# Performance work log

Hardware: AMD Instinct MI355X
Metric: run time of the kernel (lower is better)

The kernel has to match this reference:

```python
import jax, jax.numpy as jnp
import numpy as np
import math

EMBED_DIMS = 256
NUM_LANDMARKS = 40  # hard-coded k=40 in the original module
B, N = 2, 8192


def setup_inputs() -> dict:
    key = jax.random.key(0)
    ks = jax.random.split(key, 9)
    C = EMBED_DIMS
    w = lambda k: jax.random.normal(k, (C, C), dtype=jnp.float32) * 0.02
    b = lambda k: jax.random.normal(k, (C,), dtype=jnp.float32) * 0.02
    return {
        "query": jax.random.normal(ks[0], (B, N, C), dtype=jnp.float32),
        "Wq": w(ks[1]), "bq": b(ks[2]),
        "Wk": w(ks[3]), "bk": b(ks[4]),
        "Wv": w(ks[5]), "bv": b(ks[6]),
        "Wo": w(ks[7]), "bo": b(ks[8]),
    }


def reference(query, Wq, bq, Wk, bk, Wv, bv, Wo, bo):
    # key = value = identity = query (defaults in the original forward)
    C = query.shape[-1]
    scaling = math.sqrt(C)

    q = query @ Wq.T + bq  # [B, N, C]
    k = query @ Wk.T + bk
    v = query @ Wv.T + bv

    # Full similarity only to score keys: score_m[b, m] = sum_n sim_nm[b, n, m]
    sim_nm = jnp.einsum('bnc,bmc->bnm', q, k) / scaling  # [B, N, N]
    score_m = sim_nm.sum(axis=1)                          # [B, N]

    _, top_idx = jax.lax.top_k(score_m, NUM_LANDMARKS)    # [B, 40]
    selected = jnp.take_along_axis(k, top_idx[:, :, None], axis=1)  # [B, 40, C]

    sim_qn = jax.nn.softmax(jnp.einsum('bnc,bkc->bnk', q, selected) / scaling, axis=-1)  # [B, N, 40]
    sim_km = jax.nn.softmax(jnp.einsum('bmc,bkc->bmk', k, selected) / scaling, axis=-1)  # [B, N, 40]

    sim_qk = jnp.einsum('bnk,bmk->bnm', sim_qn, sim_km)   # [B, N, N]
    out = jnp.einsum('bnm,bmc->bnc', sim_qk, v)           # [B, N, C]
    out = out @ Wo.T + bo
    return query + out  # identity residual; dropouts are identity at p=0
```

## Files before the change

kernel.cpp:

```cpp
#include <hip/hip_runtime.h>
#include <cstddef>
#include <cstdint>

#define BATCH 2
#define SEQ 8192
#define CH 256
#define NLM 40
#define MROWS (BATCH * SEQ)
#define INV_SCALE 0.0625f
#define NCBLK 256

typedef unsigned short ushort_t;
typedef __attribute__((ext_vector_type(8))) short short8;
typedef __attribute__((ext_vector_type(4))) float floatx4;

__device__ __forceinline__ ushort_t f2bf(float f) {
    unsigned int u = __float_as_uint(f);
    u += 0x7FFFu + ((u >> 16) & 1u);
    return (ushort_t)(u >> 16);
}
__device__ __forceinline__ float bf2f(ushort_t u) {
    return __uint_as_float(((unsigned)u) << 16);
}

__global__ __launch_bounds__(256) void convert_colsum(const float* __restrict__ x,
                                                      ushort_t* __restrict__ xbf,
                                                      float* __restrict__ partial) {
    __shared__ float red[4][256];
    const int b = blockIdx.y;
    const int r0 = blockIdx.x * 32;
    const int t = threadIdx.x;
    const int c4 = (t & 63) * 4;
    const int rg = t >> 6;
    const float* base = x + ((size_t)b * SEQ + r0) * 256;
    ushort_t* obase = xbf + ((size_t)b * SEQ + r0) * 256;
    float4 s = {0.f, 0.f, 0.f, 0.f};
#pragma unroll
    for (int i = 0; i < 8; i++) {
        const int r = rg + i * 4;
        const float4 a = *(const float4*)&base[(size_t)r * 256 + c4];
        uint2 o;
        o.x = f2bf(a.x) | ((unsigned)f2bf(a.y) << 16);
        o.y = f2bf(a.z) | ((unsigned)f2bf(a.w) << 16);
        *(uint2*)&obase[(size_t)r * 256 + c4] = o;
        s.x += a.x; s.y += a.y; s.z += a.z; s.w += a.w;
    }
    *(float4*)&red[rg][c4] = s;
    __syncthreads();
    const float tot = red[0][t] + red[1][t] + red[2][t] + red[3][t];
    partial[((size_t)b * NCBLK + blockIdx.x) * 256 + t] = tot;
}

__global__ __launch_bounds__(1024) void ws_kernel(const float* __restrict__ partial,
                                                  const float* __restrict__ Wq,
                                                  const float* __restrict__ bq,
                                                  const float* __restrict__ Wk,
                                                  float* __restrict__ ws,
                                                  float* __restrict__ tmat) {
    const int b = blockIdx.x;
    __shared__ float xs[256];
    __shared__ float qs[256];
    __shared__ float ppart[4][256];
    const int t = threadIdx.x;
    {
        float* tz = tmat + (size_t)b * NLM * 256;
        for (int i = t; i < NLM * 256; i += 1024) tz[i] = 0.f;
    }
    {
        const int c = t & 255, qd = t >> 8;
        const float* pb = partial + ((size_t)b * NCBLK + qd * 64) * 256 + c;
        float a = 0.f;
#pragma unroll 8
        for (int i = 0; i < 64; i++) a += pb[(size_t)i * 256];
        ppart[qd][c] = a;
    }
    __syncthreads();
    if (t < 256) xs[t] = ppart[0][t] + ppart[1][t] + ppart[2][t] + ppart[3][t];
    __syncthreads();
    const int lane = t & 63, w = t >> 6;
    for (int g = 0; g < 16; g++) {
        const int o = w * 16 + g;
        const float4 wq = *(const float4*)&Wq[(size_t)o * 256 + lane * 4];
        const float4 x4 = *(const float4*)&xs[lane * 4];
        float d = wq.x * x4.x + wq.y * x4.y + wq.z * x4.z + wq.w * x4.w;
#pragma unroll
        for (int off = 32; off >= 1; off >>= 1) d += __shfl_down(d, off);
        if (lane == 0) qs[o] = d + 8192.0f * bq[o];
    }
    __syncthreads();
    const int c = t & 255, part = t >> 8;
    float a = 0.f;
    for (int o = part * 64; o < part * 64 + 64; o++)
        a += Wk[(size_t)o * 256 + c] * qs[o];
    ppart[part][c] = a;
    __syncthreads();
    if (t < 256)
        ws[b * 256 + t] = ppart[0][t] + ppart[1][t] + ppart[2][t] + ppart[3][t];
}

__global__ __launch_bounds__(256) void gemm_qkv_score(const ushort_t* __restrict__ xbf,
                                                      const float* __restrict__ Wq,
                                                      const float* __restrict__ Wk,
                                                      const float* __restrict__ Wv,
                                                      const float* __restrict__ bq,
                                                      const float* __restrict__ bk,
                                                      const float* __restrict__ bv,
                                                      ushort_t* __restrict__ qkv,
                                                      const float* __restrict__ query,
                                                      const float* __restrict__ ws,
                                                      float* __restrict__ score) {
    __shared__ __align__(16) ushort_t As[128 * 72];
    __shared__ __align__(16) ushort_t Bs[64 * 40];
    const int z = blockIdx.z;
    const int t = threadIdx.x;
    const int lane = t & 63;
    const int w = t >> 6;

    if (z == 3) {
        const int blk = blockIdx.y * 4 + blockIdx.x;
#pragma unroll
        for (int i = 0; i < 8; i++) {
            const int g = blk * 32 + i * 4 + w;
            const int b = g >> 13;
            const int m = g & 8191;
            const float4 kv = *(const float4*)&query[(size_t)g * 256 + lane * 4];
            const float4 qs = *(const float4*)&ws[b * 256 + lane * 4];
            float d = kv.x * qs.x + kv.y * qs.y + kv.z * qs.z + kv.w * qs.w;
#pragma unroll
            for (int off = 32; off >= 1; off >>= 1) d += __shfl_down(d, off);
            if (lane == 0) score[(size_t)b * SEQ + m] = d * INV_SCALE;
        }
        return;
    }

    const float* __restrict__ W = (z == 0) ? Wq : (z == 1) ? Wk : Wv;
    const float* __restrict__ bias = (z == 0) ? bq : (z == 1) ? bk : bv;
    ushort_t* __restrict__ out = qkv + (size_t)z * MROWS * 256;
    const int o0 = blockIdx.x * 64;
    const int m0 = blockIdx.y * 128;
    const int quad = lane >> 4;
    const int l16 = lane & 15;

    floatx4 acc[2][4];
#pragma unroll
    for (int rt = 0; rt < 2; rt++)
#pragma unroll
        for (int ct = 0; ct < 4; ct++) acc[rt][ct] = (floatx4){0.f, 0.f, 0.f, 0.f};

    for (int kc = 0; kc < 256; kc += 32) {
#pragma unroll
        for (int u = 0; u < 2; u++) {
            const int cid = t + u * 256;
            const int row = cid >> 2, off = cid & 3;
            *(uint4*)&As[row * 40 + off * 8] =
                *(const uint4*)&xbf[(size_t)(m0 + row) * 256 + kc + off * 8];
        }
        {
            const int row = t >> 2, off = t & 3;
            const float* wp = &W[(size_t)(o0 + row) * 256 + kc + off * 8];
            const float4 a = *(const float4*)wp;
            const float4 c = *(const float4*)(wp + 4);
            uint4 o;
            o.x = f2bf(a.x) | ((unsigned)f2bf(a.y) << 16);
            o.y = f2bf(a.z) | ((unsigned)f2bf(a.w) << 16);
            o.z = f2bf(c.x) | ((unsigned)f2bf(c.y) << 16);
            o.w = f2bf(c.z) | ((unsigned)f2bf(c.w) << 16);
            *(uint4*)&Bs[row * 40 + off * 8] = o;
        }
        __syncthreads();
        short8 a[2], b[4];
#pragma unroll
        for (int rt = 0; rt < 2; rt++)
            a[rt] = *(const short8*)&As[(w * 32 + rt * 16 + l16) * 40 + quad * 8];
#pragma unroll
        for (int ct = 0; ct < 4; ct++)
            b[ct] = *(const short8*)&Bs[(ct * 16 + l16) * 40 + quad * 8];
#pragma unroll
        for (int rt = 0; rt < 2; rt++)
#pragma unroll
            for (int ct = 0; ct < 4; ct++)
                acc[rt][ct] = __builtin_amdgcn_mfma_f32_16x16x32_bf16(
                    a[rt], b[ct], acc[rt][ct], 0, 0, 0);
        __syncthreads();
    }

#pragma unroll
    for (int rt = 0; rt < 2; rt++) {
#pragma unroll
        for (int ct = 0; ct < 4; ct++) {
            const int col = ct * 16 + l16;
            const float bb = bias[o0 + col];
#pragma unroll
            for (int reg = 0; reg < 4; reg++) {
                const int row = w * 32 + rt * 16 + quad * 4 + reg;
                As[row * 72 + col] = f2bf(acc[rt][ct][reg] + bb);
            }
        }
    }
    __syncthreads();
#pragma unroll
    for (int u = 0; u < 4; u++) {
        const int cid = t + u * 256;
        const int row = cid >> 3;
        const int off = (cid & 7) * 8;
        *(uint4*)&out[(size_t)(m0 + row) * 256 + o0 + off] =
            *(const uint4*)&As[row * 72 + off];
    }
}

__global__ __launch_bounds__(1024) void topk_gather(const float* __restrict__ score,
                                                    const ushort_t* __restrict__ kmat,
                                                    float* __restrict__ sel) {
    const int b = blockIdx.x;
    const int t = threadIdx.x;
    __shared__ unsigned hist[256];
    __shared__ unsigned wsum[64];
    __shared__ unsigned sPrefix, sMask, sRem, sNeq;
    __shared__ int sNgt;
    __shared__ int top[NLM];
    __shared__ unsigned topkey[NLM];

    unsigned key[8];
#pragma unroll
    for (int j = 0; j < 8; j++) {
        const unsigned u = __float_as_uint(score[(size_t)b * SEQ + t + j * 1024]);
        key[j] = u ^ (unsigned)(((int)u >> 31) | 0x80000000);
    }
    if (t == 0) { sPrefix = 0; sMask = 0; sRem = NLM; sNgt = 0; sNeq = 0; }

    for (int lvl = 0; lvl < 4; lvl++) {
        const int shift = 24 - 8 * lvl;
        if (t < 256) hist[t] = 0;
        __syncthreads();
        const unsigned pfx = sPrefix, msk = sMask;
#pragma unroll
        for (int j = 0; j < 8; j++)
            if (((key[j] ^ pfx) & msk) == 0)
                atomicAdd(&hist[(key[j] >> shift) & 255u], 1u);
        __syncthreads();
        if (t < 64) wsum[t] = hist[t * 4] + hist[t * 4 + 1] + hist[t * 4 + 2] + hist[t * 4 + 3];
        __syncthreads();
        if (t == 0) {
            unsigned rem = sRem, cum = 0;
            int g = 63;
            for (; g > 0; g--) { if (cum + wsum[g] >= rem) break; cum += wsum[g]; }
            int d = g * 4 + 3;
            for (; d > g * 4; d--) { if (cum + hist[d] >= rem) break; cum += hist[d]; }
            sRem = rem - cum;
            sPrefix |= ((unsigned)d) << shift;
            sMask |= 255u << shift;
        }
        __syncthreads();
    }
    const unsigned K40 = sPrefix;
    const unsigned rem = sRem;
    const int ngt = NLM - (int)rem;

#pragma unroll
    for (int j = 0; j < 8; j++) {
        if (key[j] > K40) {
            const int slot = atomicAdd(&sNgt, 1);
            top[slot] = t + j * 1024; topkey[slot] = key[j];
        } else if (key[j] == K40) {
            const unsigned e = atomicAdd(&sNeq, 1u);
            if (e < rem) {
                const int slot = ngt + (int)e;
                top[slot] = t + j * 1024; topkey[slot] = key[j];
            }
        }
    }
    __syncthreads();

    if (t < 64) {
        unsigned long long c = (t < NLM)
            ? ((((unsigned long long)(~topkey[t])) << 32) | (unsigned)top[t])
            : 0xFFFFFFFFFFFFFFFFull;
#pragma unroll
        for (int kk = 2; kk <= 64; kk <<= 1) {
#pragma unroll
            for (int j = kk >> 1; j >= 1; j >>= 1) {
                const unsigned long long o = __shfl_xor(c, j);
                const bool takeMin = ((t & kk) == 0) == ((t & j) == 0);
                const bool less = c < o;
                c = (takeMin == less) ? c : o;
            }
        }
        if (t < NLM) top[t] = (int)(c & 0xFFFFFFFFu);
    }
    __syncthreads();

    for (int f = t; f < NLM * 256; f += 1024) {
        const int j = f >> 8;
        const int cc = f & 255;
        sel[(size_t)b * NLM * 256 + f] = bf2f(kmat[((size_t)b * SEQ + top[j]) * 256 + cc]);
    }
}

__global__ __launch_bounds__(256, 4) void sim_fused(const ushort_t* __restrict__ qbf,
                                                    const ushort_t* __restrict__ kbf,
                                                    const ushort_t* __restrict__ vbf,
                                                    const float* __restrict__ sel,
                                                    float* __restrict__ simq,
                                                    float* __restrict__ tmat) {
    __shared__ __align__(16) char smem[43008];
    float (*As_)[68] = (float(*)[68])smem;
    float (*St_)[68] = (float(*)[68])(smem + 17408);
    float (*Ps)[40]  = (float(*)[40])smem;
    ushort_t* Vs     = (ushort_t*)(smem + 10240);
    const int b = blockIdx.y;
    const int n0 = blockIdx.x * 64;
    const int t = threadIdx.x;
    const int r = t >> 2, c = t & 3;
    const ushort_t* __restrict__ A = (blockIdx.z == 0) ? qbf : kbf;
    const ushort_t* __restrict__ Arow = A + ((size_t)b * SEQ + n0) * 256;
    const float* __restrict__ Sb = sel + (size_t)b * NLM * 256;

    float acc[10];
#pragma unroll
    for (int j = 0; j < 10; j++) acc[j] = 0.f;

    for (int kc = 0; kc < 256; kc += 64) {
#pragma unroll
        for (int u = 0; u < 4; u++) {
            const int f = t + u * 256;
            const int row = f >> 4;
            const int c4 = (f & 15) * 4;
            const uint2 raw = *(const uint2*)&Arow[(size_t)row * 256 + kc + c4];
            float4 fa;
            fa.x = __uint_as_float((raw.x & 0xFFFFu) << 16);
            fa.y = __uint_as_float(raw.x & 0xFFFF0000u);
            fa.z = __uint_as_float((raw.y & 0xFFFFu) << 16);
            fa.w = __uint_as_float(raw.y & 0xFFFF0000u);
            *(float4*)&As_[row][c4] = fa;
        }
#pragma unroll
        for (int u = 0; u < 3; u++) {
            const int f = t + u * 256;
            if (f < 640) {
                const int row = f >> 4;
                const int c4 = (f & 15) * 4;
                *(float4*)&St_[row][c4] = *(const float4*)&Sb[(size_t)row * 256 + kc + c4];
            }
        }
        __syncthreads();
#pragma unroll 1
        for (int i = 0; i < 64; i += 4) {
            const float4 a = *(const float4*)&As_[r][i];
#pragma unroll
            for (int j = 0; j < 10; j++) {
                const float4 s = *(const float4*)&St_[c * 10 + j][i];
                acc[j] = fmaf(a.x, s.x, acc[j]);
                acc[j] = fmaf(a.y, s.y, acc[j]);
                acc[j] = fmaf(a.z, s.z, acc[j]);
                acc[j] = fmaf(a.w, s.w, acc[j]);
            }
        }
        __syncthreads();
    }

    float mx = -1e30f;
#pragma unroll
    for (int j = 0; j < 10; j++) {
        acc[j] *= INV_SCALE;
        mx = fmaxf(mx, acc[j]);
    }
    mx = fmaxf(mx, __shfl_xor(mx, 1));
    mx = fmaxf(mx, __shfl_xor(mx, 2));
    float sum = 0.f;
#pragma unroll
    for (int j = 0; j < 10; j++) {
        acc[j] = expf(acc[j] - mx);
        sum += acc[j];
    }
    sum += __shfl_xor(sum, 1);
    sum += __shfl_xor(sum, 2);
    const float inv = 1.f / sum;
#pragma unroll
    for (int j = 0; j < 10; j++) acc[j] *= inv;

    if (blockIdx.z == 0) {
        float* __restrict__ dst = &simq[((size_t)b * SEQ + n0 + r) * NLM + c * 10];
#pragma unroll
        for (int j2 = 0; j2 < 5; j2++) {
            float2 o; o.x = acc[2 * j2]; o.y = acc[2 * j2 + 1];
            *(float2*)&dst[2 * j2] = o;
        }
        return;
    }

#pragma unroll
    for (int j = 0; j < 10; j++) Ps[r][c * 10 + j] = acc[j];
#pragma unroll
    for (int u = 0; u < 8; u++) {
        const int cid = t + u * 256;
        const int row = cid >> 5, off = (cid & 31) * 8;
        *(uint4*)&Vs[row * 256 + off] =
            *(const uint4*)&vbf[((size_t)b * SEQ + n0 + row) * 256 + off];
    }
    __syncthreads();

    float tac[40];
#pragma unroll
    for (int j = 0; j < 40; j++) tac[j] = 0.f;

#pragma unroll 2
    for (int m = 0; m < 64; m++) {
        const float vv = bf2f(Vs[m * 256 + t]);
#pragma unroll
        for (int j4 = 0; j4 < 10; j4++) {
            const float4 p = *(const float4*)&Ps[m][j4 * 4];
            tac[j4 * 4 + 0] = fmaf(p.x, vv, tac[j4 * 4 + 0]);
            tac[j4 * 4 + 1] = fmaf(p.y, vv, tac[j4 * 4 + 1]);
            tac[j4 * 4 + 2] = fmaf(p.z, vv, tac[j4 * 4 + 2]);
            tac[j4 * 4 + 3] = fmaf(p.w, vv, tac[j4 * 4 + 3]);
        }
    }
#pragma unroll
    for (int j = 0; j < 40; j++)
        atomicAdd(&tmat[(size_t)b * NLM * 256 + j * 256 + t], tac[j]);
}

__global__ __launch_bounds__(256) void out_pre_kernel(const float* __restrict__ simq,
                                                      const float* __restrict__ tmat,
                                                      ushort_t* __restrict__ outp_bf) {
    __shared__ float Pm[64][40];
    const int g0 = blockIdx.x * 64;
    const int b = g0 >> 13;
    const int t = threadIdx.x;
    float* pflat = &Pm[0][0];
    for (int f = t; f < 64 * NLM; f += 256) pflat[f] = simq[(size_t)g0 * NLM + f];
    float tc[40];
#pragma unroll
    for (int l = 0; l < 40; l++) tc[l] = tmat[(size_t)b * NLM * 256 + l * 256 + t];
    __syncthreads();
#pragma unroll 2
    for (int m = 0; m < 64; m++) {
        float a = 0.f;
#pragma unroll
        for (int j4 = 0; j4 < 10; j4++) {
            const float4 p = *(const float4*)&Pm[m][j4 * 4];
            a = fmaf(p.x, tc[j4 * 4 + 0], a);
            a = fmaf(p.y, tc[j4 * 4 + 1], a);
            a = fmaf(p.z, tc[j4 * 4 + 2], a);
            a = fmaf(p.w, tc[j4 * 4 + 3], a);
        }
        outp_bf[((size_t)g0 + m) * 256 + t] = f2bf(a);
    }
}

__global__ __launch_bounds__(256) void gemm_out(const ushort_t* __restrict__ Abf,
                                                const float* __restrict__ Wo,
                                                const float* __restrict__ bias,
                                                const float* __restrict__ resid,
                                                float* __restrict__ out) {
    __shared__ __align__(16) char smem[128 * 68 * 4];
    ushort_t* As = (ushort_t*)smem;
    ushort_t* Bs = (ushort_t*)(smem + 128 * 40 * 2);
    float* Ft = (float*)smem;
    const int t = threadIdx.x;
    const int o0 = blockIdx.x * 64;
    const int m0 = blockIdx.y * 128;
    const int lane = t & 63;
    const int w = t >> 6;
    const int quad = lane >> 4;
    const int l16 = lane & 15;

    floatx4 acc[2][4];
#pragma unroll
    for (int rt = 0; rt < 2; rt++)
#pragma unroll
        for (int ct = 0; ct < 4; ct++) acc[rt][ct] = (floatx4){0.f, 0.f, 0.f, 0.f};

    for (int kc = 0; kc < 256; kc += 32) {
#pragma unroll
        for (int u = 0; u < 2; u++) {
            const int cid = t + u * 256;
            const int row = cid >> 2, off = cid & 3;
            *(uint4*)&As[row * 40 + off * 8] =
                *(const uint4*)&Abf[(size_t)(m0 + row) * 256 + kc + off * 8];
        }
        {
            const int row = t >> 2, off = t & 3;
            const float* wp = &Wo[(size_t)(o0 + row) * 256 + kc + off * 8];
            const float4 a = *(const float4*)wp;
            const float4 c = *(const float4*)(wp + 4);
            uint4 o;
            o.x = f2bf(a.x) | ((unsigned)f2bf(a.y) << 16);
            o.y = f2bf(a.z) | ((unsigned)f2bf(a.w) << 16);
            o.z = f2bf(c.x) | ((unsigned)f2bf(c.y) << 16);
            o.w = f2bf(c.z) | ((unsigned)f2bf(c.w) << 16);
            *(uint4*)&Bs[row * 40 + off * 8] = o;
        }
        __syncthreads();
        short8 a[2], b[4];
#pragma unroll
        for (int rt = 0; rt < 2; rt++)
            a[rt] = *(const short8*)&As[(w * 32 + rt * 16 + l16) * 40 + quad * 8];
#pragma unroll
        for (int ct = 0; ct < 4; ct++)
            b[ct] = *(const short8*)&Bs[(ct * 16 + l16) * 40 + quad * 8];
#pragma unroll
        for (int rt = 0; rt < 2; rt++)
#pragma unroll
            for (int ct = 0; ct < 4; ct++)
                acc[rt][ct] = __builtin_amdgcn_mfma_f32_16x16x32_bf16(
                    a[rt], b[ct], acc[rt][ct], 0, 0, 0);
        __syncthreads();
    }

#pragma unroll
    for (int rt = 0; rt < 2; rt++) {
#pragma unroll
        for (int ct = 0; ct < 4; ct++) {
            const int col = ct * 16 + l16;
            const float bb = bias[o0 + col];
#pragma unroll
            for (int reg = 0; reg < 4; reg++) {
                const int row = w * 32 + rt * 16 + quad * 4 + reg;
                Ft[row * 68 + col] = acc[rt][ct][reg] + bb;
            }
        }
    }
    __syncthreads();
#pragma unroll
    for (int u = 0; u < 8; u++) {
        const int cid = t + u * 256;
        const int row = cid >> 4;
        const int off = (cid & 15) * 4;
        const float4 v = *(const float4*)&Ft[row * 68 + off];
        const float4 r4 = *(const float4*)&resid[(size_t)(m0 + row) * 256 + o0 + off];
        float4 o;
        o.x = v.x + r4.x; o.y = v.y + r4.y; o.z = v.z + r4.z; o.w = v.w + r4.w;
        *(float4*)&out[(size_t)(m0 + row) * 256 + o0 + off] = o;
    }
}

extern "C" void kernel_launch(void* const* d_in, const int* in_sizes, int n_in,
                              void* d_out, int out_size, void* d_ws, size_t ws_size,
                              hipStream_t stream) {
    const float* query = (const float*)d_in[0];
    const float* Wq = (const float*)d_in[1];
    const float* bq = (const float*)d_in[2];
    const float* Wk = (const float*)d_in[3];
    const float* bk = (const float*)d_in[4];
    const float* Wv = (const float*)d_in[5];
    const float* bv = (const float*)d_in[6];
    const float* Wo = (const float*)d_in[7];
    const float* bo = (const float*)d_in[8];
    float* out = (float*)d_out;

    char* p = (char*)d_ws;
    float* simq  = (float*)p;            p += (size_t)MROWS * NLM * 4;
    float* sel   = (float*)p;            p += (size_t)BATCH * NLM * 256 * 4;
    float* tmat  = (float*)p;            p += (size_t)BATCH * NLM * 256 * 4;
    float* partial = (float*)p;          p += (size_t)BATCH * NCBLK * 256 * 4;
    float* ws    = (float*)p;            p += (size_t)BATCH * 256 * 4;
    float* score = (float*)p;            p += (size_t)BATCH * SEQ * 4;
    ushort_t* qkv = (ushort_t*)p;        p += (size_t)3 * MROWS * 256 * 2;
    ushort_t* xbf = (ushort_t*)p;        p += (size_t)MROWS * 256 * 2;
    ushort_t* qbf = qkv;
    ushort_t* kbf = qkv + (size_t)MROWS * 256;
    ushort_t* vbf = qkv + (size_t)2 * MROWS * 256;
    ushort_t* outp_bf = xbf;

    const dim3 blk(256);

    convert_colsum<<<dim3(SEQ / 32, BATCH), blk, 0, stream>>>(query, xbf, partial);
    ws_kernel<<<dim3(BATCH), dim3(1024), 0, stream>>>(partial, Wq, bq, Wk, ws, tmat);

    gemm_qkv_score<<<dim3(4, MROWS / 128, 4), blk, 0, stream>>>(
        xbf, Wq, Wk, Wv, bq, bk, bv, qkv, query, ws, score);

    topk_gather<<<dim3(BATCH), dim3(1024), 0, stream>>>(score, kbf, sel);

    sim_fused<<<dim3(SEQ / 64, BATCH, 2), blk, 0, stream>>>(qbf, kbf, vbf, sel, simq, tmat);

    out_pre_kernel<<<dim3(MROWS / 64), blk, 0, stream>>>(simq, tmat, outp_bf);
    gemm_out<<<dim3(4, MROWS / 128), blk, 0, stream>>>(outp_bf, Wo, bo, query, out);
}
```

Measured before the change: 205.3 us.

## Compute landmark similarity logits with bf16 MFMA instead of scalar FP32 FMA

The landmark-logit step in sim_fused now uses 16x16x32 bf16 MFMA instructions. Operands are read straight from global memory, replacing the LDS-staged fp32 FMA loop. The gathered landmark keys are stored as bf16 and zero-padded to 48 rows so three 16-column tiles cover the 40 landmarks, with the padding masked out of the softmax. This removes the LDS staging, bf16-to-fp32 unpacking and scalar FMA cost. In exchange it adds cross-lane shuffles for the row softmax, uncoalesced scattered simq stores, and global-memory operand loads with no LDS reuse.

Result: faster. 196.7 us (-4.2%).

```diff
diff --git a/kernel.cpp b/kernel.cpp
--- a/kernel.cpp
+++ b/kernel.cpp
@@ -6,6 +6,7 @@
 #define SEQ 8192
 #define CH 256
 #define NLM 40
+#define NLMP 48
 #define MROWS (BATCH * SEQ)
 #define INV_SCALE 0.0625f
 #define NCBLK 256
@@ -210,7 +211,7 @@
 
 __global__ __launch_bounds__(1024) void topk_gather(const float* __restrict__ score,
                                                     const ushort_t* __restrict__ kmat,
-                                                    float* __restrict__ sel) {
+                                                    ushort_t* __restrict__ sel) {
     const int b = blockIdx.x;
     const int t = threadIdx.x;
     __shared__ unsigned hist[256];
@@ -289,107 +290,94 @@
     }
     __syncthreads();
 
-    for (int f = t; f < NLM * 256; f += 1024) {
+    for (int f = t; f < NLMP * 256; f += 1024) {
         const int j = f >> 8;
         const int cc = f & 255;
-        sel[(size_t)b * NLM * 256 + f] = bf2f(kmat[((size_t)b * SEQ + top[j]) * 256 + cc]);
+        sel[(size_t)b * NLMP * 256 + f] =
+            (j < NLM) ? kmat[((size_t)b * SEQ + top[j]) * 256 + cc] : (ushort_t)0;
     }
 }
 
 __global__ __launch_bounds__(256, 4) void sim_fused(const ushort_t* __restrict__ qbf,
                                                     const ushort_t* __restrict__ kbf,
                                                     const ushort_t* __restrict__ vbf,
-                                                    const float* __restrict__ sel,
+                                                    const ushort_t* __restrict__ sel,
                                                     float* __restrict__ simq,
                                                     float* __restrict__ tmat) {
     __shared__ __align__(16) char smem[43008];
-    float (*As_)[68] = (float(*)[68])smem;
-    float (*St_)[68] = (float(*)[68])(smem + 17408);
     float (*Ps)[40]  = (float(*)[40])smem;
     ushort_t* Vs     = (ushort_t*)(smem + 10240);
     const int b = blockIdx.y;
     const int n0 = blockIdx.x * 64;
     const int t = threadIdx.x;
-    const int r = t >> 2, c = t & 3;
+    const int lane = t & 63;
+    const int w = t >> 6;
+    const int quad = lane >> 4;
+    const int l16 = lane & 15;
     const ushort_t* __restrict__ A = (blockIdx.z == 0) ? qbf : kbf;
-    const ushort_t* __restrict__ Arow = A + ((size_t)b * SEQ + n0) * 256;
-    const float* __restrict__ Sb = sel + (size_t)b * NLM * 256;
-
-    float acc[10];
-#pragma unroll
-    for (int j = 0; j < 10; j++) acc[j] = 0.f;
-
-    for (int kc = 0; kc < 256; kc += 64) {
-#pragma unroll
-        for (int u = 0; u < 4; u++) {
-            const int f = t + u * 256;
-            const int row = f >> 4;
-            const int c4 = (f & 15) * 4;
-            const uint2 raw = *(const uint2*)&Arow[(size_t)row * 256 + kc + c4];
-            float4 fa;
-            fa.x = __uint_as_float((raw.x & 0xFFFFu) << 16);
-            fa.y = __uint_as_float(raw.x & 0xFFFF0000u);
-            fa.z = __uint_as_float((raw.y & 0xFFFFu) << 16);
-            fa.w = __uint_as_float(raw.y & 0xFFFF0000u);
-            *(float4*)&As_[row][c4] = fa;
-        }
-#pragma unroll
-        for (int u = 0; u < 3; u++) {
-            const int f = t + u * 256;
-            if (f < 640) {
-                const int row = f >> 4;
-                const int c4 = (f & 15) * 4;
-                *(float4*)&St_[row][c4] = *(const float4*)&Sb[(size_t)row * 256 + kc + c4];
-            }
-        }
-        __syncthreads();
-#pragma unroll 1
-        for (int i = 0; i < 64; i += 4) {
-            const float4 a = *(const float4*)&As_[r][i];
-#pragma unroll
-            for (int j = 0; j < 10; j++) {
-                const float4 s = *(const float4*)&St_[c * 10 + j][i];
-                acc[j] = fmaf(a.x, s.x, acc[j]);
-                acc[j] = fmaf(a.y, s.y, acc[j]);
-                acc[j] = fmaf(a.z, s.z, acc[j]);
-                acc[j] = fmaf(a.w, s.w, acc[j]);
-            }
-        }
-        __syncthreads();
-    }
-
-    float mx = -1e30f;
-#pragma unroll
-    for (int j = 0; j < 10; j++) {
-        acc[j] *= INV_SCALE;
-        mx = fmaxf(mx, acc[j]);
-    }
-    mx = fmaxf(mx, __shfl_xor(mx, 1));
-    mx = fmaxf(mx, __shfl_xor(mx, 2));
-    float sum = 0.f;
-#pragma unroll
-    for (int j = 0; j < 10; j++) {
-        acc[j] = expf(acc[j] - mx);
-        sum += acc[j];
-    }
-    sum += __shfl_xor(sum, 1);
-    sum += __shfl_xor(sum, 2);
-    const float inv = 1.f / sum;
-#pragma unroll
-    for (int j = 0; j < 10; j++) acc[j] *= inv;
-
+    const ushort_t* __restrict__ Arow = A + ((size_t)b * SEQ + n0 + w * 16 + l16) * 256;
+    const ushort_t* __restrict__ Sb = sel + (size_t)b * NLMP * 256 + (size_t)l16 * 256;
+
+    floatx4 acc[3];
+#pragma unroll
+    for (int ct = 0; ct < 3; ct++) acc[ct] = (floatx4){0.f, 0.f, 0.f, 0.f};
+
+#pragma unroll
+    for (int ks = 0; ks < 8; ks++) {
+        const int ko = ks * 32 + quad * 8;
+        const short8 a  = *(const short8*)&Arow[ko];
+        const short8 b0 = *(const short8*)&Sb[ko];
+        const short8 b1 = *(const short8*)&Sb[16 * 256 + ko];
+        const short8 b2 = *(const short8*)&Sb[32 * 256 + ko];
+        acc[0] = __builtin_amdgcn_mfma_f32_16x16x32_bf16(a, b0, acc[0], 0, 0, 0);
+        acc[1] = __builtin_amdgcn_mfma_f32_16x16x32_bf16(a, b1, acc[1], 0, 0, 0);
+        acc[2] = __builtin_amdgcn_mfma_f32_16x16x32_bf16(a, b2, acc[2], 0, 0, 0);
+    }
+
+    const bool v2ok = (l16 < 8);
+    float p0[4], p1[4], p2[4];
+#pragma unroll
+    for (int reg = 0; reg < 4; reg++) {
+        const float l0 = acc[0][reg] * INV_SCALE;
+        const float l1 = acc[1][reg] * INV_SCALE;
+        const float l2 = acc[2][reg] * INV_SCALE;
+        float m = fmaxf(l0, l1);
+        if (v2ok) m = fmaxf(m, l2);
+        m = fmaxf(m, __shfl_xor(m, 1));
+        m = fmaxf(m, __shfl_xor(m, 2));
+        m = fmaxf(m, __shfl_xor(m, 4));
+        m = fmaxf(m, __shfl_xor(m, 8));
+        const float e0 = expf(l0 - m);
+        const float e1 = expf(l1 - m);
+        const float e2 = v2ok ? expf(l2 - m) : 0.f;
+        float s = e0 + e1 + e2;
+        s += __shfl_xor(s, 1);
+        s += __shfl_xor(s, 2);
+        s += __shfl_xor(s, 4);
+        s += __shfl_xor(s, 8);
+        const float inv = 1.f / s;
+        p0[reg] = e0 * inv; p1[reg] = e1 * inv; p2[reg] = e2 * inv;
+    }
+
+    const int row0 = w * 16 + quad * 4;
     if (blockIdx.z == 0) {
-        float* __restrict__ dst = &simq[((size_t)b * SEQ + n0 + r) * NLM + c * 10];
-#pragma unroll
-        for (int j2 = 0; j2 < 5; j2++) {
-            float2 o; o.x = acc[2 * j2]; o.y = acc[2 * j2 + 1];
-            *(float2*)&dst[2 * j2] = o;
+        float* __restrict__ dst = &simq[((size_t)b * SEQ + n0 + row0) * NLM];
+#pragma unroll
+        for (int reg = 0; reg < 4; reg++) {
+            float* __restrict__ d2 = dst + reg * NLM;
+            d2[l16] = p0[reg];
+            d2[16 + l16] = p1[reg];
+            if (v2ok) d2[32 + l16] = p2[reg];
         }
         return;
     }
 
 #pragma unroll
-    for (int j = 0; j < 10; j++) Ps[r][c * 10 + j] = acc[j];
+    for (int reg = 0; reg < 4; reg++) {
+        Ps[row0 + reg][l16] = p0[reg];
+        Ps[row0 + reg][16 + l16] = p1[reg];
+        if (v2ok) Ps[row0 + reg][32 + l16] = p2[reg];
+    }
 #pragma unroll
     for (int u = 0; u < 8; u++) {
         const int cid = t + u * 256;
@@ -551,7 +539,7 @@
 
     char* p = (char*)d_ws;
     float* simq  = (float*)p;            p += (size_t)MROWS * NLM * 4;
-    float* sel   = (float*)p;            p += (size_t)BATCH * NLM * 256 * 4;
+    ushort_t* selbf = (ushort_t*)p;      p += (size_t)BATCH * NLMP * 256 * 2;
     float* tmat  = (float*)p;            p += (size_t)BATCH * NLM * 256 * 4;
     float* partial = (float*)p;          p += (size_t)BATCH * NCBLK * 256 * 4;
     float* ws    = (float*)p;            p += (size_t)BATCH * 256 * 4;
@@ -571,9 +559,9 @@
     gemm_qkv_score<<<dim3(4, MROWS / 128, 4), blk, 0, stream>>>(
         xbf, Wq, Wk, Wv, bq, bk, bv, qkv, query, ws, score);
 
-    topk_gather<<<dim3(BATCH), dim3(1024), 0, stream>>>(score, kbf, sel);
-
-    sim_fused<<<dim3(SEQ / 64, BATCH, 2), blk, 0, stream>>>(qbf, kbf, vbf, sel, simq, tmat);
+    topk_gather<<<dim3(BATCH), dim3(1024), 0, stream>>>(score, kbf, selbf);
+
+    sim_fused<<<dim3(SEQ / 64, BATCH, 2), blk, 0, stream>>>(qbf, kbf, vbf, selbf, simq, tmat);
 
     out_pre_kernel<<<dim3(MROWS / 64), blk, 0, stream>>>(simq, tmat, outp_bf);
     gemm_out<<<dim3(4, MROWS / 128), blk, 0, stream>>>(outp_bf, Wo, bo, query, out);
```
